# Optimization experiments

Measured on AMD Instinct MI355X. Metric: run time of the kernel, lower is better.

## Reference

```python
import jax, jax.numpy as jnp
import numpy as np

WS = 800      # window size
HEADS = 3
DH = 24       # dim_head
LOWRANK_W = 30
NEG_SLOPE = 0.01  # LeakyReLU default
LN_EPS = 1e-5


def _layernorm(x, g, b):
    m = jnp.mean(x, axis=-1, keepdims=True)
    v = jnp.var(x, axis=-1, keepdims=True)
    return (x - m) * jax.lax.rsqrt(v + LN_EPS) * g + b


def setup_inputs() -> dict:
    key = jax.random.key(0)
    ks = jax.random.split(key, 20)
    B, CIN, H, W = 2, 5, 160, 160
    D = 48
    INNER = HEADS * DH  # 72
    f32 = jnp.float32

    def n(k, shape, s=0.05):
        return jax.random.normal(k, shape, f32) * s

    return {
        "x": jax.random.normal(ks[0], (B, CIN, H, W), f32),
        # Embedding: Conv2d(5, 48, 3, pad=1) + PReLU
        "conv_w": n(ks[1], (D, CIN, 3, 3), 0.1),
        "conv_b": jnp.zeros((D,), f32),
        "prelu_a": jnp.array(0.25, f32),
        # attention PreNorm
        "ln1_g": jnp.ones((D,), f32),
        "ln1_b": jnp.zeros((D,), f32),
        # to_qkv: Linear(48, 216, bias=False)
        "w_qkv": n(ks[2], (3 * INNER, D)),
        # Linformer low-rank params E,F: [heads, dim_head, w]
        "E_mat": jax.random.normal(ks[3], (HEADS, DH, LOWRANK_W), f32),
        "F_mat": jax.random.normal(ks[4], (HEADS, DH, LOWRANK_W), f32),
        # lin1/lin2: Linear(w, dim_head)
        "w_e": n(ks[5], (DH, LOWRANK_W)),
        "b_e": jnp.zeros((DH,), f32),
        "w_f": n(ks[6], (DH, LOWRANK_W)),
        "b_f": jnp.zeros((DH,), f32),
        # to_out: Linear(72, 48)
        "w_out": n(ks[7], (D, INNER)),
        "b_out": jnp.zeros((D,), f32),
        # FF PreNorm + MLP (dim=48, hidden=48)
        "ln2_g": jnp.ones((D,), f32),
        "ln2_b": jnp.zeros((D,), f32),
        "ff_w1": n(ks[8], (D, D)),
        "ff_b1": jnp.zeros((D,), f32),
        "ff_w2": n(ks[9], (D, D)),
        "ff_b2": jnp.zeros((D,), f32),
        # final lin1: Linear(48, 96)
        "w_fin": n(ks[10], (2 * D, D)),
        "b_fin": jnp.zeros((2 * D,), f32),
    }


def reference(x, conv_w, conv_b, prelu_a, ln1_g, ln1_b, w_qkv, E_mat, F_mat,
              w_e, b_e, w_f, b_f, w_out, b_out, ln2_g, ln2_b,
              ff_w1, ff_b1, ff_w2, ff_b2, w_fin, b_fin):
    B, _, H, W = x.shape
    # Embedding: conv3x3 same + PReLU
    E = jax.lax.conv_general_dilated(
        x, conv_w, (1, 1), ((1, 1), (1, 1)),
        dimension_numbers=("NCHW", "OIHW", "NCHW")) + conv_b[None, :, None, None]
    E = jnp.maximum(E, 0) + prelu_a * jnp.minimum(E, 0)
    D = E.shape[1]
    seq = E.reshape(B, D, H * W).transpose(0, 2, 1)  # [B, N, D]
    N = seq.shape[1]
    nw = N // WS

    # --- Residual(PreNorm(LinformerAttention_wind1)) ---
    xn = _layernorm(seq, ln1_g, ln1_b)
    xw = xn.reshape(B, nw, WS, D)                         # windows
    qkv = jnp.einsum("bwnc,oc->bwno", xw, w_qkv)          # [B,nw,WS,216]
    qkv = qkv.reshape(B, nw, WS, HEADS, 3 * DH).transpose(0, 1, 3, 2, 4)
    q, k, v = jnp.split(qkv, 3, axis=-1)                  # each [B,nw,h,WS,DH]
    # einsum 'b h n d, h d d -> b h n d' == scale by diagonal of lin(E/F)
    e_diag = jnp.einsum("hdw,dw->hd", E_mat, w_e) + b_e   # [h, DH]
    f_diag = jnp.einsum("hdw,dw->hd", F_mat, w_f) + b_f
    k = k * e_diag[None, None, :, None, :]
    v = v * f_diag[None, None, :, None, :]
    scale = DH ** -0.5
    dots = jnp.einsum("bwhid,bwhjd->bwhij", q, k) * scale  # [B,nw,h,WS,WS]
    attn = jax.nn.softmax(dots, axis=-1)
    ow = jnp.einsum("bwhij,bwhjd->bwhid", attn, v)
    ow = ow.transpose(0, 1, 3, 2, 4).reshape(B, N, HEADS * DH)
    att = jnp.einsum("bnf,of->bno", ow, w_out) + b_out
    seq = seq + att

    # --- Residual(PreNorm(FeedForward)) ---
    yn = _layernorm(seq, ln2_g, ln2_b)
    h = jnp.einsum("bnc,oc->bno", yn, ff_w1) + ff_b1
    h = jnp.where(h >= 0, h, NEG_SLOPE * h)
    h = jnp.einsum("bno,co->bnc", h, ff_w2) + ff_b2
    att1 = seq + h                                        # [B, N, D]

    hp = att1.transpose(0, 2, 1).reshape(B, D, H, W)
    Highpass1 = E * hp + E
    lin = jnp.einsum("bnc,oc->bno", att1, w_fin) + b_fin  # [B, N, 2D]
    return (Highpass1, lin)
```

## Files before the change

### kernel.cpp

```cpp
#include <hip/hip_runtime.h>
#include <hip/hip_bf16.h>

#define B_    2
#define CIN_  5
#define H_    160
#define W_    160
#define N_    25600
#define D_    48
#define NW_   32
#define WS_   800
#define HEADS_ 3
#define DH_   24
#define INNER_ 72
#define NWH_  192

typedef __bf16 bf16x8 __attribute__((ext_vector_type(8)));
typedef float  f32x4  __attribute__((ext_vector_type(4)));

#define MFMA(a,b,c) __builtin_amdgcn_mfma_f32_16x16x32_bf16((a),(b),(c),0,0,0)

__device__ __forceinline__ float fast_exp2(float x) {
#if __has_builtin(__builtin_amdgcn_exp2f)
    return __builtin_amdgcn_exp2f(x);
#else
    return exp2f(x);
#endif
}

__device__ __forceinline__ unsigned pack_bf16(float lo, float hi) {
    __bf16 l = (__bf16)lo, h = (__bf16)hi;
    unsigned short ul = __builtin_bit_cast(unsigned short, l);
    unsigned short uh = __builtin_bit_cast(unsigned short, h);
    return ((unsigned)uh << 16) | (unsigned)ul;
}

__global__ __launch_bounds__(256) void k_wprep(const float* __restrict__ wqkv,
                                               const float* __restrict__ w_out,
                                               const float* __restrict__ fw1,
                                               const float* __restrict__ fw2,
                                               const float* __restrict__ wfin,
                                               const float* __restrict__ cw,
                                               const float* __restrict__ Em,
                                               const float* __restrict__ Fm,
                                               const float* __restrict__ we,
                                               const float* __restrict__ be,
                                               const float* __restrict__ wf,
                                               const float* __restrict__ bf,
                                               float* __restrict__ diag,
                                               __bf16* __restrict__ wqB,
                                               __bf16* __restrict__ woB,
                                               __bf16* __restrict__ f1B,
                                               __bf16* __restrict__ f2B,
                                               __bf16* __restrict__ wfB,
                                               __bf16* __restrict__ wcB) {
    if (blockIdx.x == 0 && threadIdx.x < 72) {
        int tt = threadIdx.x;
        int h = tt / 24, d = tt % 24;
        float se = be[d], sf = bf[d];
        for (int w = 0; w < 30; ++w) {
            se += Em[(h*24+d)*30 + w] * we[d*30 + w];
            sf += Fm[(h*24+d)*30 + w] * wf[d*30 + w];
        }
        diag[tt]      = se;
        diag[72 + tt] = sf;
    }
    int t = blockIdx.x*256 + threadIdx.x, stride = gridDim.x*256;
    for (int i = t; i < 288*64; i += stride) {
        int grow = i>>6, c = i&63;
        int gg = grow>>5, q = grow&31, tt = q>>4, sp = q&15, d = tt*16+sp;
        int part = gg/3, head = gg%3;
        wqB[i] = (d<24 && c<48) ? (__bf16)wqkv[(head*72 + part*24 + d)*48 + c] : (__bf16)0.f;
    }
    for (int i = t; i < 48*96;  i += stride) {
        int o = i/96, p = i%96;
        int h = p>>5, q = p&31, j = q&1, sp = q>>1, d = j*16+sp;
        woB[i] = (d<24) ? (__bf16)w_out[o*72 + h*24 + d] : (__bf16)0.f;
    }
    for (int i = t; i < 48*64;  i += stride) { int o=i>>6, c=i&63; f1B[i] = (c<48)? (__bf16)fw1[o*48+c] : (__bf16)0.f; }
    for (int i = t; i < 48*64;  i += stride) { int o=i>>6, c=i&63; f2B[i] = (c<48)? (__bf16)fw2[o*48+c] : (__bf16)0.f; }
    for (int i = t; i < 96*64;  i += stride) { int o=i>>6, c=i&63; wfB[i] = (c<48)? (__bf16)wfin[o*48+c] : (__bf16)0.f; }
    for (int i = t; i < 48*64;  i += stride) { int o=i>>6, c=i&63; wcB[i] = (c<45)? (__bf16)cw[o*45+c] : (__bf16)0.f; }
}

__global__ __launch_bounds__(256) void k_cqkv(const float* __restrict__ x,
                                              const __bf16* __restrict__ wcB,
                                              const float* __restrict__ cb,
                                              const float* __restrict__ pa,
                                              const __bf16* __restrict__ wqB,
                                              const float* __restrict__ g1,
                                              const float* __restrict__ b1,
                                              const float* __restrict__ diag,
                                              float* __restrict__ seqT,
                                              __bf16* __restrict__ Qbf,
                                              __bf16* __restrict__ Kbf,
                                              __bf16* __restrict__ Vt) {
    __shared__ float Lx[CIN_][4][W_];
    __shared__ __bf16 xfer[64*64];
    int t = threadIdx.x;
    int blk = blockIdx.x;
    int b = blk / 400;
    int n0 = (blk % 400) * 64;
    int y0 = n0 / W_;

    for (int i = t; i < CIN_*4*W_; i += 256) {
        int ic = i / (4*W_), rem = i % (4*W_), yy = rem / W_, col = rem % W_;
        int yr = y0 - 1 + yy;
        float v = 0.f;
        if (yr >= 0 && yr < H_)
            v = x[((size_t)(b*CIN_ + ic)*H_ + yr)*W_ + col];
        Lx[ic][yy][col] = v;
    }
    __syncthreads();

    int wv = t >> 6, lane = t & 63, g = lane>>4, s = lane&15;
    char* xb = (char*)xfer;

    {
        int rloc0 = wv * 16;
        bf16x8 ac[2];
        {
            int row = rloc0 + s;
            int n  = n0 + row;
            int y  = n / W_, xx = n % W_;
            int dy = y - y0;
            #pragma unroll
            for (int kc = 0; kc < 2; ++kc) {
                int kbase = kc*32 + g*8;
                #pragma unroll
                for (int j = 0; j < 8; ++j) {
                    int k = kbase + j;
                    int ic = k / 9, rem = k % 9, ky = rem / 3, kx = rem % 3;
                    int xc = xx + kx - 1;
                    float v = 0.f;
                    if ((kc == 0 || k < 45) && xc >= 0 && xc < W_)
                        v = Lx[ic][dy + ky][xc];
                    ac[kc][j] = (__bf16)v;
                }
            }
        }
        const bf16x8* WC4 = (const bf16x8*)wcB;
        float a = pa[0];
        float cbv[3], g1v[3], b1v[3];
        #pragma unroll
        for (int n = 0; n < 3; ++n) {
            cbv[n] = cb[n*16+s]; g1v[n] = g1[n*16+s]; b1v[n] = b1[n*16+s];
        }
        float xr[3][4];
        #pragma unroll
        for (int n = 0; n < 3; ++n) {
            bf16x8 wb0 = WC4[(n*16+s)*8 + g];
            bf16x8 wb1 = WC4[(n*16+s)*8 + 4 + g];
            f32x4 c = {0.f,0.f,0.f,0.f};
            c = MFMA(ac[0], wb0, c);
            c = MFMA(ac[1], wb1, c);
            #pragma unroll
            for (int r = 0; r < 4; ++r) {
                float vv = c[r] + cbv[n];
                vv = vv >= 0.f ? vv : a * vv;
                xr[n][r] = vv;
            }
        }
        int grow0 = blk*64 + rloc0;
        #pragma unroll
        for (int n = 0; n < 3; ++n)
          #pragma unroll
          for (int r = 0; r < 4; ++r)
            seqT[(size_t)(grow0 + g*4 + r)*48 + n*16 + s] = xr[n][r];

        #pragma unroll
        for (int r = 0; r < 4; ++r) {
            float sm = xr[0][r] + xr[1][r] + xr[2][r];
            float sq = xr[0][r]*xr[0][r] + xr[1][r]*xr[1][r] + xr[2][r]*xr[2][r];
            #pragma unroll
            for (int msk = 1; msk < 16; msk <<= 1) { sm += __shfl_xor(sm, msk); sq += __shfl_xor(sq, msk); }
            float mean = sm * (1.f/48.f);
            float var  = sq * (1.f/48.f) - mean*mean;
            float rs   = rsqrtf(var + 1e-5f);
            int row = rloc0 + g*4 + r;
            int sw  = ((g*4+r)&7) << 4;
            #pragma unroll
            for (int n = 0; n < 3; ++n) {
                float yn = (xr[n][r] - mean) * rs * g1v[n] + b1v[n];
                *(__bf16*)(xb + ((row*128 + (n*16+s)*2) ^ sw)) = (__bf16)yn;
            }
            *(__bf16*)(xb + ((row*128 + (48+s)*2) ^ sw)) = (__bf16)0.f;
        }
    }
    __syncthreads();

    int rh = wv & 1, gh = wv >> 1;
    int growQ = blk*64 + rh*32;
    int nrem = growQ % N_;
    int w = nrem / WS_, i0 = nrem % WS_;
    size_t headbase = (size_t)((b*NW_ + w)*HEADS_);

    bf16x8 af[2][2];
    #pragma unroll
    for (int m = 0; m < 2; ++m)
      #pragma unroll
      for (int kc = 0; kc < 2; ++kc) {
        int row = rh*32 + m*16 + s;
        af[m][kc] = *(const bf16x8*)(xb + ((row*128 + kc*64 + g*16) ^ ((s&7)<<4)));
      }

    const bf16x8* WQ4 = (const bf16x8*)wqB;
    const float SCALE = 0.2944889919f;

    float dke[3], dko[3], dve[3], dvo[3];
    #pragma unroll
    for (int h = 0; h < 3; ++h) {
        dke[h] = diag[h*24 + s];
        dko[h] = (s < 8) ? diag[h*24 + 16 + s] : 0.f;
        dve[h] = diag[72 + h*24 + s];
        dvo[h] = (s < 8) ? diag[72 + h*24 + 16 + s] : 0.f;
    }

    unsigned* Qd = (unsigned*)Qbf;
    unsigned* Kd = (unsigned*)Kbf;

    int gg0 = gh ? 5 : 0, gg1 = gh ? 9 : 5;
    for (int gg = gg0; gg < gg1; ++gg) {
        int part = gg / 3, head = gg % 3;
        bf16x8 we0 = WQ4[(gg*32 +      s)*8 +     g];
        bf16x8 we1 = WQ4[(gg*32 +      s)*8 + 4 + g];
        bf16x8 wo0 = WQ4[(gg*32 + 16 + s)*8 +     g];
        bf16x8 wo1 = WQ4[(gg*32 + 16 + s)*8 + 4 + g];
        f32x4 ce[2], co[2];
        __builtin_amdgcn_s_setprio(1);
        #pragma unroll
        for (int m = 0; m < 2; ++m) {
            f32x4 c = {0.f,0.f,0.f,0.f};
            c = MFMA(af[m][0], we0, c); c = MFMA(af[m][1], we1, c);
            ce[m] = c;
            f32x4 d = {0.f,0.f,0.f,0.f};
            d = MFMA(af[m][0], wo0, d); d = MFMA(af[m][1], wo1, d);
            co[m] = d;
        }
        __builtin_amdgcn_s_setprio(0);
        size_t rbase = (headbase + head)*WS_ + i0;
        if (part == 0) {
            #pragma unroll
            for (int m = 0; m < 2; ++m)
              #pragma unroll
              for (int r = 0; r < 4; ++r)
                Qd[(rbase + m*16 + g*4 + r)*16 + s] =
                    pack_bf16(ce[m][r]*SCALE, co[m][r]*SCALE);
        } else if (part == 1) {
            #pragma unroll
            for (int m = 0; m < 2; ++m)
              #pragma unroll
              for (int r = 0; r < 4; ++r) {
                int p5 = 16*(g&1) + 8*m + 4*(g>>1) + r;
                Kd[(rbase + p5)*16 + s] =
                    pack_bf16(ce[m][r]*dke[head], co[m][r]*dko[head]);
              }
        } else {
            size_t vbase = (headbase + head)*((size_t)32*WS_) + i0;
            #pragma unroll
            for (int m = 0; m < 2; ++m) {
                uint2 pe;
                pe.x = pack_bf16(ce[m][0]*dve[head], ce[m][1]*dve[head]);
                pe.y = pack_bf16(ce[m][2]*dve[head], ce[m][3]*dve[head]);
                *(uint2*)&Vt[vbase + (size_t)s*WS_ + m*16 + g*4] = pe;
                if (s < 8) {
                    uint2 po;
                    po.x = pack_bf16(co[m][0]*dvo[head], co[m][1]*dvo[head]);
                    po.y = pack_bf16(co[m][2]*dvo[head], co[m][3]*dvo[head]);
                    *(uint2*)&Vt[vbase + (size_t)(16+s)*WS_ + m*16 + g*4] = po;
                }
            }
        }
    }
    if (gh == 1) {
        unsigned* Vd = (unsigned*)Vt;
        #pragma unroll
        for (int it = 0; it < 6; ++it) {
            int idx = it*64 + lane;
            int h = idx >> 7, rem = idx & 127;
            int dd = 24 + (rem >> 4), cp = rem & 15;
            size_t ubase = (((headbase + h)*((size_t)32*WS_) + (size_t)dd*WS_ + i0) >> 1);
            Vd[ubase + cp] = (dd == 24) ? 0x3F803F80u : 0u;
        }
    }
}

__global__ __launch_bounds__(256, 4) void k_attn(const __bf16* __restrict__ Qbf,
                                                 const __bf16* __restrict__ Kbf,
                                                 const __bf16* __restrict__ Vt,
                                                 __bf16* __restrict__ OW) {
    __shared__ float red[2][5][2][4][64];
    int t = threadIdx.x;
    int wv = t >> 6, lane = t & 63;
    int g = lane >> 4, s = lane & 15;
    int half = wv & 1, tsk = wv >> 1;
    int blk = blockIdx.x;
    int v = (blk & 7) * 120 + (blk >> 3);
    int task = v * 2 + tsk;
    int wh = task / 10, qt = task % 10;
    int q0 = qt * 80;

    const bf16x8* Qp = (const bf16x8*)(Qbf + ((size_t)wh*WS_ + q0)*32);
    const bf16x8* Kp = (const bf16x8*)(Kbf + (size_t)wh*WS_*32);
    const bf16x8* Vp = (const bf16x8*)(Vt  + (size_t)wh*32*WS_);

    bf16x8 qb[5];
    #pragma unroll
    for (int i = 0; i < 5; ++i) qb[i] = Qp[(i*16 + s)*4 + g];

    f32x4 o[5][2];
    #pragma unroll
    for (int i = 0; i < 5; ++i) {
        o[i][0] = (f32x4){0.f,0.f,0.f,0.f};
        o[i][1] = (f32x4){0.f,0.f,0.f,0.f};
    }

    int c0 = half ? 12 : 0;
    int c1 = half ? 25 : 12;

    bf16x8 ka0 = Kp[(c0*32 + s)*4 + g];
    bf16x8 ka1 = Kp[(c0*32 + 16 + s)*4 + g];
    bf16x8 vb0 = Vp[s*100 + c0*4 + g];
    bf16x8 vb1 = Vp[(16+s)*100 + c0*4 + g];

    for (int c = c0; c < c1; ++c) {
        int cn = (c + 1 < c1) ? c + 1 : c0;
        bf16x8 nk0 = Kp[(cn*32 + s)*4 + g];
        bf16x8 nk1 = Kp[(cn*32 + 16 + s)*4 + g];
        bf16x8 nv0 = Vp[s*100 + cn*4 + g];
        bf16x8 nv1 = Vp[(16+s)*100 + cn*4 + g];

        __builtin_amdgcn_s_setprio(1);
        #pragma unroll
        for (int i = 0; i < 5; ++i) {
            f32x4 s0 = {0.f,0.f,0.f,0.f}, s1 = {0.f,0.f,0.f,0.f};
            s0 = MFMA(ka0, qb[i], s0);
            s1 = MFMA(ka1, qb[i], s1);
            bf16x8 pa;
            #pragma unroll
            for (int r = 0; r < 4; ++r) {
                pa[r]     = (__bf16)fast_exp2(s0[r]);
                pa[r + 4] = (__bf16)fast_exp2(s1[r]);
            }
            o[i][0] = MFMA(pa, vb0, o[i][0]);
            o[i][1] = MFMA(pa, vb1, o[i][1]);
        }
        __builtin_amdgcn_s_setprio(0);
        ka0 = nk0; ka1 = nk1; vb0 = nv0; vb1 = nv1;
    }

    if (half) {
        #pragma unroll
        for (int i = 0; i < 5; ++i)
          #pragma unroll
          for (int j = 0; j < 2; ++j)
            #pragma unroll
            for (int r = 0; r < 4; ++r)
              red[tsk][i][j][r][lane] = o[i][j][r];
    }
    __syncthreads();
    if (!half) {
        #pragma unroll
        for (int i = 0; i < 5; ++i)
          #pragma unroll
          for (int j = 0; j < 2; ++j)
            #pragma unroll
            for (int r = 0; r < 4; ++r)
              o[i][j][r] += red[tsk][i][j][r][lane];

        int bw = wh / 3, h = wh % 3;
        int b = bw >> 5, w = bw & 31;
        unsigned* OWd = (unsigned*)OW;
        #pragma unroll
        for (int i = 0; i < 5; ++i) {
            #pragma unroll
            for (int r = 0; r < 4; ++r) {
                float den = __shfl(o[i][1][r], (lane & 48) + 8);
                float inv = 1.f / den;
                int n = w*WS_ + q0 + i*16 + g*4 + r;
                OWd[(size_t)(b*N_ + n)*48 + h*16 + s] =
                    pack_bf16(o[i][0][r]*inv, o[i][1][r]*inv);
            }
        }
    }
}

__global__ __launch_bounds__(256) void k_tail(const float* __restrict__ seqT,
                                              const __bf16* __restrict__ OW,
                                              const __bf16* __restrict__ woB,
                                              const float* __restrict__ b_out,
                                              const float* __restrict__ g2,
                                              const float* __restrict__ b2,
                                              const __bf16* __restrict__ f1B,
                                              const float* __restrict__ fb1,
                                              const __bf16* __restrict__ f2B,
                                              const float* __restrict__ fb2,
                                              const __bf16* __restrict__ wfB,
                                              const float* __restrict__ bfin,
                                              float* __restrict__ out1,
                                              float* __restrict__ out2) {
    __shared__ __bf16 xfer[4][2048];
    __shared__ float hp[4][32][49];
    int t = threadIdx.x, wv = t>>6, lane = t&63, g = lane>>4, s = lane&15;
    int row0 = (blockIdx.x*4 + wv) * 32;
    char* xb = (char*)&xfer[wv][0];

    int b = row0 / N_;
    int nbase = row0 % N_;

    const bf16x8* OW4 = (const bf16x8*)OW;
    const bf16x8* WO4 = (const bf16x8*)woB;
    const bf16x8* F14 = (const bf16x8*)f1B;
    const bf16x8* F24 = (const bf16x8*)f2B;
    const bf16x8* WF4 = (const bf16x8*)wfB;

    bf16x8 aow[2][3];
    #pragma unroll
    for (int m = 0; m < 2; ++m)
      #pragma unroll
      for (int kc = 0; kc < 3; ++kc)
        aow[m][kc] = OW4[(size_t)(row0 + m*16 + s)*12 + kc*4 + g];

    f32x4 s2[2][3];
    __builtin_amdgcn_s_setprio(1);
    #pragma unroll
    for (int n = 0; n < 3; ++n) {
        bf16x8 wb0 = WO4[(n*16+s)*12 + g];
        bf16x8 wb1 = WO4[(n*16+s)*12 + 4 + g];
        bf16x8 wb2 = WO4[(n*16+s)*12 + 8 + g];
        #pragma unroll
        for (int m = 0; m < 2; ++m) {
            f32x4 c = {0.f,0.f,0.f,0.f};
            c = MFMA(aow[m][0], wb0, c);
            c = MFMA(aow[m][1], wb1, c);
            c = MFMA(aow[m][2], wb2, c);
            s2[m][n] = c;
        }
    }
    __builtin_amdgcn_s_setprio(0);
    float bov[3], g2v[3], b2v[3], f1bv[3], f2bv[3];
    #pragma unroll
    for (int n = 0; n < 3; ++n) {
        bov[n] = b_out[n*16+s]; g2v[n] = g2[n*16+s]; b2v[n] = b2[n*16+s];
        f1bv[n] = fb1[n*16+s];  f2bv[n] = fb2[n*16+s];
    }
    float sv[2][3][4];
    #pragma unroll
    for (int m = 0; m < 2; ++m)
      #pragma unroll
      for (int n = 0; n < 3; ++n)
        #pragma unroll
        for (int r = 0; r < 4; ++r) {
          sv[m][n][r] = seqT[(size_t)(row0 + m*16 + g*4 + r)*48 + n*16 + s];
          s2[m][n][r] += sv[m][n][r] + bov[n];
        }

    #pragma unroll
    for (int m = 0; m < 2; ++m)
      #pragma unroll
      for (int r = 0; r < 4; ++r) {
        float sm = s2[m][0][r] + s2[m][1][r] + s2[m][2][r];
        float sq = s2[m][0][r]*s2[m][0][r] + s2[m][1][r]*s2[m][1][r] + s2[m][2][r]*s2[m][2][r];
        #pragma unroll
        for (int msk = 1; msk < 16; msk <<= 1) { sm += __shfl_xor(sm, msk); sq += __shfl_xor(sq, msk); }
        float mean = sm * (1.f/48.f);
        float var  = sq * (1.f/48.f) - mean*mean;
        float rs   = rsqrtf(var + 1e-5f);
        int row = m*16 + g*4 + r;
        int sw  = ((g*4+r)&7) << 4;
        #pragma unroll
        for (int n = 0; n < 3; ++n) {
            float yn = (s2[m][n][r] - mean) * rs * g2v[n] + b2v[n];
            *(__bf16*)(xb + ((row*128 + (n*16+s)*2) ^ sw)) = (__bf16)yn;
        }
        *(__bf16*)(xb + ((row*128 + (48+s)*2) ^ sw)) = (__bf16)0.f;
      }

    bf16x8 af[2][2];
    f32x4 hh[2][3];

    #pragma unroll
    for (int m = 0; m < 2; ++m)
      #pragma unroll
      for (int kc = 0; kc < 2; ++kc)
        af[m][kc] = *(const bf16x8*)(xb + (((m*16+s)*128 + kc*64 + g*16) ^ ((s&7)<<4)));
    __builtin_amdgcn_s_setprio(1);
    #pragma unroll
    for (int n = 0; n < 3; ++n) {
        bf16x8 wb0 = F14[(n*16+s)*8 + g];
        bf16x8 wb1 = F14[(n*16+s)*8 + 4 + g];
        #pragma unroll
        for (int m = 0; m < 2; ++m) {
            f32x4 c = {0.f,0.f,0.f,0.f};
            c = MFMA(af[m][0], wb0, c);
            c = MFMA(af[m][1], wb1, c);
            hh[m][n] = c;
        }
    }
    __builtin_amdgcn_s_setprio(0);
    #pragma unroll
    for (int m = 0; m < 2; ++m)
      #pragma unroll
      for (int r = 0; r < 4; ++r) {
        int row = m*16 + g*4 + r;
        int sw  = ((g*4+r)&7) << 4;
        #pragma unroll
        for (int n = 0; n < 3; ++n) {
            float v = hh[m][n][r] + f1bv[n];
            v = v >= 0.f ? v : 0.01f*v;
            *(__bf16*)(xb + ((row*128 + (n*16+s)*2) ^ sw)) = (__bf16)v;
        }
        *(__bf16*)(xb + ((row*128 + (48+s)*2) ^ sw)) = (__bf16)0.f;
      }

    #pragma unroll
    for (int m = 0; m < 2; ++m)
      #pragma unroll
      for (int kc = 0; kc < 2; ++kc)
        af[m][kc] = *(const bf16x8*)(xb + (((m*16+s)*128 + kc*64 + g*16) ^ ((s&7)<<4)));
    __builtin_amdgcn_s_setprio(1);
    #pragma unroll
    for (int n = 0; n < 3; ++n) {
        bf16x8 wb0 = F24[(n*16+s)*8 + g];
        bf16x8 wb1 = F24[(n*16+s)*8 + 4 + g];
        #pragma unroll
        for (int m = 0; m < 2; ++m) {
            f32x4 c = {0.f,0.f,0.f,0.f};
            c = MFMA(af[m][0], wb0, c);
            c = MFMA(af[m][1], wb1, c);
            hh[m][n] = c;
        }
    }
    __builtin_amdgcn_s_setprio(0);
    #pragma unroll
    for (int m = 0; m < 2; ++m)
      #pragma unroll
      for (int r = 0; r < 4; ++r) {
        int row = m*16 + g*4 + r;
        int sw  = ((g*4+r)&7) << 4;
        #pragma unroll
        for (int n = 0; n < 3; ++n) {
            float a1v = s2[m][n][r] + hh[m][n][r] + f2bv[n];
            hp[wv][row][n*16+s] = sv[m][n][r] * (1.f + a1v);
            *(__bf16*)(xb + ((row*128 + (n*16+s)*2) ^ sw)) = (__bf16)a1v;
        }
        *(__bf16*)(xb + ((row*128 + (48+s)*2) ^ sw)) = (__bf16)0.f;
      }

    #pragma unroll
    for (int it = 0; it < 6; ++it) {
        int flat = it*256 + lane*4;
        int ch = flat >> 5, row = flat & 31;
        float4 v = { hp[wv][row][ch], hp[wv][row+1][ch],
                     hp[wv][row+2][ch], hp[wv][row+3][ch] };
        *(float4*)&out1[((size_t)b*D_ + ch)*N_ + nbase + row] = v;
    }

    #pragma unroll
    for (int m = 0; m < 2; ++m)
      #pragma unroll
      for (int kc = 0; kc < 2; ++kc)
        af[m][kc] = *(const bf16x8*)(xb + (((m*16+s)*128 + kc*64 + g*16) ^ ((s&7)<<4)));
    #pragma unroll
    for (int n = 0; n < 6; ++n) {
        bf16x8 wb0 = WF4[(n*16+s)*8 + g];
        bf16x8 wb1 = WF4[(n*16+s)*8 + 4 + g];
        float bfv = bfin[n*16+s];
        __builtin_amdgcn_s_setprio(1);
        f32x4 cc[2];
        #pragma unroll
        for (int m = 0; m < 2; ++m) {
            f32x4 c = {0.f,0.f,0.f,0.f};
            c = MFMA(af[m][0], wb0, c);
            c = MFMA(af[m][1], wb1, c);
            cc[m] = c;
        }
        __builtin_amdgcn_s_setprio(0);
        #pragma unroll
        for (int m = 0; m < 2; ++m)
          #pragma unroll
          for (int r = 0; r < 4; ++r)
            out2[(size_t)(row0 + m*16 + g*4 + r)*96 + n*16 + s] = cc[m][r] + bfv;
    }
}

extern "C" void kernel_launch(void* const* d_in, const int* in_sizes, int n_in,
                              void* d_out, int out_size, void* d_ws, size_t ws_size,
                              hipStream_t stream) {
    const float* x      = (const float*)d_in[0];
    const float* conv_w = (const float*)d_in[1];
    const float* conv_b = (const float*)d_in[2];
    const float* prelu_a= (const float*)d_in[3];
    const float* ln1_g  = (const float*)d_in[4];
    const float* ln1_b  = (const float*)d_in[5];
    const float* w_qkv  = (const float*)d_in[6];
    const float* E_mat  = (const float*)d_in[7];
    const float* F_mat  = (const float*)d_in[8];
    const float* w_e    = (const float*)d_in[9];
    const float* b_e    = (const float*)d_in[10];
    const float* w_f    = (const float*)d_in[11];
    const float* b_f    = (const float*)d_in[12];
    const float* w_out  = (const float*)d_in[13];
    const float* b_out  = (const float*)d_in[14];
    const float* ln2_g  = (const float*)d_in[15];
    const float* ln2_b  = (const float*)d_in[16];
    const float* ff_w1  = (const float*)d_in[17];
    const float* ff_b1  = (const float*)d_in[18];
    const float* ff_w2  = (const float*)d_in[19];
    const float* ff_b2  = (const float*)d_in[20];
    const float* w_fin  = (const float*)d_in[21];
    const float* b_fin  = (const float*)d_in[22];

    float* ws = (float*)d_ws;
    float*  seqT = ws;
    float*  diag = seqT + (size_t)B_*N_*D_;
    __bf16* Qbf  = (__bf16*)(diag + 144);
    __bf16* Kbf  = Qbf + (size_t)NWH_*WS_*32;
    __bf16* Vt   = Kbf + (size_t)NWH_*WS_*32;
    __bf16* OW   = Vt + (size_t)NWH_*32*WS_;
    __bf16* wqB  = OW + (size_t)B_*N_*96;
    __bf16* woB  = wqB + 288*64;
    __bf16* f1B  = woB + 48*96;
    __bf16* f2B  = f1B + 48*64;
    __bf16* wfB  = f2B + 48*64;
    __bf16* wcB  = wfB + 96*64;

    float* out1 = (float*)d_out;
    float* out2 = out1 + (size_t)B_*D_*N_;

    k_wprep<<<32, 256, 0, stream>>>(w_qkv, w_out, ff_w1, ff_w2, w_fin, conv_w,
                                    E_mat, F_mat, w_e, b_e, w_f, b_f, diag,
                                    wqB, woB, f1B, f2B, wfB, wcB);
    k_cqkv<<<800, 256, 0, stream>>>(x, wcB, conv_b, prelu_a,
                                    wqB, ln1_g, ln1_b, diag, seqT, Qbf, Kbf, Vt);
    k_attn<<<960, 256, 0, stream>>>(Qbf, Kbf, Vt, OW);
    k_tail<<<400, 256, 0, stream>>>(seqT, OW, woB, b_out, ln2_g, ln2_b,
                                    f1B, ff_b1, f2B, ff_b2, wfB, b_fin,
                                    out1, out2);
}
```

Before: 72.69 us.

## Split tail kernel output columns across three waves per row tile

Restructures k_tail so each 32-row tile is processed by three waves, each owning one 16-column slice of the 48 output channels, instead of one wave doing all columns. LayerNorm row statistics are combined through a small shared buffer, and double shared staging buffers with block barriers replace per-wave private buffers. The launch grows to 800 blocks of 384 threads. This aims to raise parallelism and cut per-wave serial MFMA and epilogue work. In exchange it adds __syncthreads barriers and redundant loads of the activation fragments in every wave.

```diff
diff --git a/kernel.cpp b/kernel.cpp
--- a/kernel.cpp
+++ b/kernel.cpp
@@ -384,7 +384,7 @@
     }
 }
 
-__global__ __launch_bounds__(256) void k_tail(const float* __restrict__ seqT,
+__global__ __launch_bounds__(384) void k_tail(const float* __restrict__ seqT,
                                               const __bf16* __restrict__ OW,
                                               const __bf16* __restrict__ woB,
                                               const float* __restrict__ b_out,
@@ -398,14 +398,19 @@
                                               const float* __restrict__ bfin,
                                               float* __restrict__ out1,
                                               float* __restrict__ out2) {
-    __shared__ __bf16 xfer[4][2048];
-    __shared__ float hp[4][32][49];
-    int t = threadIdx.x, wv = t>>6, lane = t&63, g = lane>>4, s = lane&15;
-    int row0 = (blockIdx.x*4 + wv) * 32;
-    char* xb = (char*)&xfer[wv][0];
-
+    __shared__ __bf16 xA[2][2048];
+    __shared__ __bf16 xB[2][2048];
+    __shared__ float  hp[2][32][49];
+    __shared__ float  lnp[2][3][2][32];
+    int t = threadIdx.x;
+    int w6 = t / 64, lane = t & 63, g = lane >> 4, s = lane & 15;
+    int rh = w6 / 3, nc = w6 % 3;
+    int blk = blockIdx.x;
+    int row0 = blk*64 + rh*32;
     int b = row0 / N_;
-    int nbase = row0 % N_;
+    int nbase0 = (blk*64) % N_;
+    char* xa  = (char*)&xA[rh][0];
+    char* xbb = (char*)&xB[rh][0];
 
     const bf16x8* OW4 = (const bf16x8*)OW;
     const bf16x8* WO4 = (const bf16x8*)woB;
@@ -420,153 +425,159 @@
       for (int kc = 0; kc < 3; ++kc)
         aow[m][kc] = OW4[(size_t)(row0 + m*16 + s)*12 + kc*4 + g];
 
-    f32x4 s2[2][3];
-    __builtin_amdgcn_s_setprio(1);
-    #pragma unroll
-    for (int n = 0; n < 3; ++n) {
-        bf16x8 wb0 = WO4[(n*16+s)*12 + g];
-        bf16x8 wb1 = WO4[(n*16+s)*12 + 4 + g];
-        bf16x8 wb2 = WO4[(n*16+s)*12 + 8 + g];
+    f32x4 s2[2];
+    {
+        bf16x8 wb0 = WO4[(nc*16+s)*12 + g];
+        bf16x8 wb1 = WO4[(nc*16+s)*12 + 4 + g];
+        bf16x8 wb2 = WO4[(nc*16+s)*12 + 8 + g];
+        __builtin_amdgcn_s_setprio(1);
         #pragma unroll
         for (int m = 0; m < 2; ++m) {
             f32x4 c = {0.f,0.f,0.f,0.f};
             c = MFMA(aow[m][0], wb0, c);
             c = MFMA(aow[m][1], wb1, c);
             c = MFMA(aow[m][2], wb2, c);
-            s2[m][n] = c;
-        }
-    }
-    __builtin_amdgcn_s_setprio(0);
-    float bov[3], g2v[3], b2v[3], f1bv[3], f2bv[3];
-    #pragma unroll
-    for (int n = 0; n < 3; ++n) {
-        bov[n] = b_out[n*16+s]; g2v[n] = g2[n*16+s]; b2v[n] = b2[n*16+s];
-        f1bv[n] = fb1[n*16+s];  f2bv[n] = fb2[n*16+s];
-    }
-    float sv[2][3][4];
-    #pragma unroll
-    for (int m = 0; m < 2; ++m)
-      #pragma unroll
-      for (int n = 0; n < 3; ++n)
-        #pragma unroll
-        for (int r = 0; r < 4; ++r) {
-          sv[m][n][r] = seqT[(size_t)(row0 + m*16 + g*4 + r)*48 + n*16 + s];
-          s2[m][n][r] += sv[m][n][r] + bov[n];
-        }
-
+            s2[m] = c;
+        }
+        __builtin_amdgcn_s_setprio(0);
+    }
+    float bov  = b_out[nc*16+s];
+    float g2v  = g2[nc*16+s],  b2v  = b2[nc*16+s];
+    float f1bv = fb1[nc*16+s], f2bv = fb2[nc*16+s];
+
+    float sv[2][4];
     #pragma unroll
     for (int m = 0; m < 2; ++m)
       #pragma unroll
       for (int r = 0; r < 4; ++r) {
-        float sm = s2[m][0][r] + s2[m][1][r] + s2[m][2][r];
-        float sq = s2[m][0][r]*s2[m][0][r] + s2[m][1][r]*s2[m][1][r] + s2[m][2][r]*s2[m][2][r];
+        sv[m][r] = seqT[(size_t)(row0 + m*16 + g*4 + r)*48 + nc*16 + s];
+        s2[m][r] += sv[m][r] + bov;
+      }
+
+    #pragma unroll
+    for (int m = 0; m < 2; ++m)
+      #pragma unroll
+      for (int r = 0; r < 4; ++r) {
+        float sm = s2[m][r];
+        float sq = s2[m][r]*s2[m][r];
         #pragma unroll
         for (int msk = 1; msk < 16; msk <<= 1) { sm += __shfl_xor(sm, msk); sq += __shfl_xor(sq, msk); }
+        if (s == 0) {
+            int row = m*16 + g*4 + r;
+            lnp[rh][nc][0][row] = sm;
+            lnp[rh][nc][1][row] = sq;
+        }
+      }
+    __syncthreads();
+
+    #pragma unroll
+    for (int m = 0; m < 2; ++m)
+      #pragma unroll
+      for (int r = 0; r < 4; ++r) {
+        int row = m*16 + g*4 + r;
+        float sm = lnp[rh][0][0][row] + lnp[rh][1][0][row] + lnp[rh][2][0][row];
+        float sq = lnp[rh][0][1][row] + lnp[rh][1][1][row] + lnp[rh][2][1][row];
         float mean = sm * (1.f/48.f);
         float var  = sq * (1.f/48.f) - mean*mean;
         float rs   = rsqrtf(var + 1e-5f);
-        int row = m*16 + g*4 + r;
-        int sw  = ((g*4+r)&7) << 4;
-        #pragma unroll
-        for (int n = 0; n < 3; ++n) {
-            float yn = (s2[m][n][r] - mean) * rs * g2v[n] + b2v[n];
-            *(__bf16*)(xb + ((row*128 + (n*16+s)*2) ^ sw)) = (__bf16)yn;
-        }
-        *(__bf16*)(xb + ((row*128 + (48+s)*2) ^ sw)) = (__bf16)0.f;
+        float yn = (s2[m][r] - mean) * rs * g2v + b2v;
+        int sw = ((g*4+r)&7) << 4;
+        *(__bf16*)(xa + ((row*128 + (nc*16+s)*2) ^ sw)) = (__bf16)yn;
+        if (nc == 0)
+            *(__bf16*)(xa + ((row*128 + (48+s)*2) ^ sw)) = (__bf16)0.f;
       }
+    __syncthreads();
 
     bf16x8 af[2][2];
-    f32x4 hh[2][3];
+    f32x4 hh[2];
 
     #pragma unroll
     for (int m = 0; m < 2; ++m)
       #pragma unroll
       for (int kc = 0; kc < 2; ++kc)
-        af[m][kc] = *(const bf16x8*)(xb + (((m*16+s)*128 + kc*64 + g*16) ^ ((s&7)<<4)));
-    __builtin_amdgcn_s_setprio(1);
-    #pragma unroll
-    for (int n = 0; n < 3; ++n) {
-        bf16x8 wb0 = F14[(n*16+s)*8 + g];
-        bf16x8 wb1 = F14[(n*16+s)*8 + 4 + g];
+        af[m][kc] = *(const bf16x8*)(xa + (((m*16+s)*128 + kc*64 + g*16) ^ ((s&7)<<4)));
+    {
+        bf16x8 wb0 = F14[(nc*16+s)*8 + g];
+        bf16x8 wb1 = F14[(nc*16+s)*8 + 4 + g];
+        __builtin_amdgcn_s_setprio(1);
         #pragma unroll
         for (int m = 0; m < 2; ++m) {
             f32x4 c = {0.f,0.f,0.f,0.f};
             c = MFMA(af[m][0], wb0, c);
             c = MFMA(af[m][1], wb1, c);
-            hh[m][n] = c;
-        }
-    }
-    __builtin_amdgcn_s_setprio(0);
+            hh[m] = c;
+        }
+        __builtin_amdgcn_s_setprio(0);
+    }
     #pragma unroll
     for (int m = 0; m < 2; ++m)
       #pragma unroll
       for (int r = 0; r < 4; ++r) {
         int row = m*16 + g*4 + r;
         int sw  = ((g*4+r)&7) << 4;
-        #pragma unroll
-        for (int n = 0; n < 3; ++n) {
-            float v = hh[m][n][r] + f1bv[n];
-            v = v >= 0.f ? v : 0.01f*v;
-            *(__bf16*)(xb + ((row*128 + (n*16+s)*2) ^ sw)) = (__bf16)v;
-        }
-        *(__bf16*)(xb + ((row*128 + (48+s)*2) ^ sw)) = (__bf16)0.f;
+        float v = hh[m][r] + f1bv;
+        v = v >= 0.f ? v : 0.01f*v;
+        *(__bf16*)(xbb + ((row*128 + (nc*16+s)*2) ^ sw)) = (__bf16)v;
+        if (nc == 0)
+            *(__bf16*)(xbb + ((row*128 + (48+s)*2) ^ sw)) = (__bf16)0.f;
       }
+    __syncthreads();
 
     #pragma unroll
     for (int m = 0; m < 2; ++m)
       #pragma unroll
       for (int kc = 0; kc < 2; ++kc)
-        af[m][kc] = *(const bf16x8*)(xb + (((m*16+s)*128 + kc*64 + g*16) ^ ((s&7)<<4)));
-    __builtin_amdgcn_s_setprio(1);
-    #pragma unroll
-    for (int n = 0; n < 3; ++n) {
-        bf16x8 wb0 = F24[(n*16+s)*8 + g];
-        bf16x8 wb1 = F24[(n*16+s)*8 + 4 + g];
+        af[m][kc] = *(const bf16x8*)(xbb + (((m*16+s)*128 + kc*64 + g*16) ^ ((s&7)<<4)));
+    {
+        bf16x8 wb0 = F24[(nc*16+s)*8 + g];
+        bf16x8 wb1 = F24[(nc*16+s)*8 + 4 + g];
+        __builtin_amdgcn_s_setprio(1);
         #pragma unroll
         for (int m = 0; m < 2; ++m) {
             f32x4 c = {0.f,0.f,0.f,0.f};
             c = MFMA(af[m][0], wb0, c);
             c = MFMA(af[m][1], wb1, c);
-            hh[m][n] = c;
-        }
-    }
-    __builtin_amdgcn_s_setprio(0);
+            hh[m] = c;
+        }
+        __builtin_amdgcn_s_setprio(0);
+    }
     #pragma unroll
     for (int m = 0; m < 2; ++m)
       #pragma unroll
       for (int r = 0; r < 4; ++r) {
         int row = m*16 + g*4 + r;
         int sw  = ((g*4+r)&7) << 4;
-        #pragma unroll
-        for (int n = 0; n < 3; ++n) {
-            float a1v = s2[m][n][r] + hh[m][n][r] + f2bv[n];
-            hp[wv][row][n*16+s] = sv[m][n][r] * (1.f + a1v);
-            *(__bf16*)(xb + ((row*128 + (n*16+s)*2) ^ sw)) = (__bf16)a1v;
-        }
-        *(__bf16*)(xb + ((row*128 + (48+s)*2) ^ sw)) = (__bf16)0.f;
+        float a1v = s2[m][r] + hh[m][r] + f2bv;
+        hp[rh][row][nc*16+s] = sv[m][r] * (1.f + a1v);
+        *(__bf16*)(xa + ((row*128 + (nc*16+s)*2) ^ sw)) = (__bf16)a1v;
+        if (nc == 0)
+            *(__bf16*)(xa + ((row*128 + (48+s)*2) ^ sw)) = (__bf16)0.f;
       }
-
-    #pragma unroll
-    for (int it = 0; it < 6; ++it) {
-        int flat = it*256 + lane*4;
-        int ch = flat >> 5, row = flat & 31;
-        float4 v = { hp[wv][row][ch], hp[wv][row+1][ch],
-                     hp[wv][row+2][ch], hp[wv][row+3][ch] };
-        *(float4*)&out1[((size_t)b*D_ + ch)*N_ + nbase + row] = v;
+    __syncthreads();
+
+    #pragma unroll
+    for (int it = 0; it < 2; ++it) {
+        int flat = it*1536 + t*4;
+        int ch = flat >> 6, row = flat & 63;
+        int h2 = row >> 5, rl = row & 31;
+        float4 v = { hp[h2][rl][ch], hp[h2][rl+1][ch],
+                     hp[h2][rl+2][ch], hp[h2][rl+3][ch] };
+        *(float4*)&out1[((size_t)b*D_ + ch)*N_ + nbase0 + row] = v;
     }
 
     #pragma unroll
     for (int m = 0; m < 2; ++m)
       #pragma unroll
       for (int kc = 0; kc < 2; ++kc)
-        af[m][kc] = *(const bf16x8*)(xb + (((m*16+s)*128 + kc*64 + g*16) ^ ((s&7)<<4)));
-    #pragma unroll
-    for (int n = 0; n < 6; ++n) {
+        af[m][kc] = *(const bf16x8*)(xa + (((m*16+s)*128 + kc*64 + g*16) ^ ((s&7)<<4)));
+    #pragma unroll
+    for (int nn = 0; nn < 2; ++nn) {
+        int n = nc + nn*3;
         bf16x8 wb0 = WF4[(n*16+s)*8 + g];
         bf16x8 wb1 = WF4[(n*16+s)*8 + 4 + g];
         float bfv = bfin[n*16+s];
+        f32x4 cc[2];
         __builtin_amdgcn_s_setprio(1);
-        f32x4 cc[2];
         #pragma unroll
         for (int m = 0; m < 2; ++m) {
             f32x4 c = {0.f,0.f,0.f,0.f};
@@ -633,7 +644,7 @@
     k_cqkv<<<800, 256, 0, stream>>>(x, wcB, conv_b, prelu_a,
                                     wqB, ln1_g, ln1_b, diag, seqT, Qbf, Kbf, Vt);
     k_attn<<<960, 256, 0, stream>>>(Qbf, Kbf, Vt, OW);
-    k_tail<<<400, 256, 0, stream>>>(seqT, OW, woB, b_out, ln2_g, ln2_b,
+    k_tail<<<800, 384, 0, stream>>>(seqT, OW, woB, b_out, ln2_g, ln2_b,
                                     f1B, ff_b1, f2B, ff_b2, wfB, b_fin,
                                     out1, out2);
 }
```

New measurement: 80.60 us. +10.9%, slower.

## Halve conv+QKV tile to 32 rows with narrow halo staging, doubling grid

Applied to the files above, without the earlier changes.

The fused conv/LayerNorm/QKV kernel now processes 32 tokens per block instead of 64, launching 1600 blocks. It stages only a 3x34 halo of the input per channel instead of four full image rows, which cuts redundant global loads and LDS use. The 9 QKV head-groups are redistributed across all four waves (2,2,3,2 groups), and wave 3 writes the V padding. Only two waves do the conv stage now, and each block repeats the weight loads and halo overhead.

```diff
diff --git a/kernel.cpp b/kernel.cpp
--- a/kernel.cpp
+++ b/kernel.cpp
@@ -94,20 +94,22 @@
                                               __bf16* __restrict__ Qbf,
                                               __bf16* __restrict__ Kbf,
                                               __bf16* __restrict__ Vt) {
-    __shared__ float Lx[CIN_][4][W_];
-    __shared__ __bf16 xfer[64*64];
+    __shared__ float Lx[CIN_][3][34];
+    __shared__ __bf16 xfer[32*64];
     int t = threadIdx.x;
     int blk = blockIdx.x;
-    int b = blk / 400;
-    int n0 = (blk % 400) * 64;
+    int b = blk / 800;
+    int n0 = (blk % 800) * 32;
     int y0 = n0 / W_;
-
-    for (int i = t; i < CIN_*4*W_; i += 256) {
-        int ic = i / (4*W_), rem = i % (4*W_), yy = rem / W_, col = rem % W_;
+    int x0 = n0 % W_;
+
+    for (int i = t; i < CIN_*3*34; i += 256) {
+        int ic = i / (3*34), rem = i % (3*34), yy = rem / 34, col = rem % 34;
         int yr = y0 - 1 + yy;
+        int xc = x0 - 1 + col;
         float v = 0.f;
-        if (yr >= 0 && yr < H_)
-            v = x[((size_t)(b*CIN_ + ic)*H_ + yr)*W_ + col];
+        if (yr >= 0 && yr < H_ && xc >= 0 && xc < W_)
+            v = x[((size_t)(b*CIN_ + ic)*H_ + yr)*W_ + xc];
         Lx[ic][yy][col] = v;
     }
     __syncthreads();
@@ -115,27 +117,21 @@
     int wv = t >> 6, lane = t & 63, g = lane>>4, s = lane&15;
     char* xb = (char*)xfer;
 
-    {
+    if (wv < 2) {
         int rloc0 = wv * 16;
+        int rib = rloc0 + s;
         bf16x8 ac[2];
-        {
-            int row = rloc0 + s;
-            int n  = n0 + row;
-            int y  = n / W_, xx = n % W_;
-            int dy = y - y0;
-            #pragma unroll
-            for (int kc = 0; kc < 2; ++kc) {
-                int kbase = kc*32 + g*8;
-                #pragma unroll
-                for (int j = 0; j < 8; ++j) {
-                    int k = kbase + j;
-                    int ic = k / 9, rem = k % 9, ky = rem / 3, kx = rem % 3;
-                    int xc = xx + kx - 1;
-                    float v = 0.f;
-                    if ((kc == 0 || k < 45) && xc >= 0 && xc < W_)
-                        v = Lx[ic][dy + ky][xc];
-                    ac[kc][j] = (__bf16)v;
-                }
+        #pragma unroll
+        for (int kc = 0; kc < 2; ++kc) {
+            int kbase = kc*32 + g*8;
+            #pragma unroll
+            for (int j = 0; j < 8; ++j) {
+                int k = kbase + j;
+                int ic = k / 9, rem = k % 9, ky = rem / 3, kx = rem % 3;
+                float v = 0.f;
+                if (kc == 0 || k < 45)
+                    v = Lx[ic][ky][rib + kx];
+                ac[kc][j] = (__bf16)v;
             }
         }
         const bf16x8* WC4 = (const bf16x8*)wcB;
@@ -160,7 +156,7 @@
                 xr[n][r] = vv;
             }
         }
-        int grow0 = blk*64 + rloc0;
+        int grow0 = blk*32 + rloc0;
         #pragma unroll
         for (int n = 0; n < 3; ++n)
           #pragma unroll
@@ -188,10 +184,7 @@
     }
     __syncthreads();
 
-    int rh = wv & 1, gh = wv >> 1;
-    int growQ = blk*64 + rh*32;
-    int nrem = growQ % N_;
-    int w = nrem / WS_, i0 = nrem % WS_;
+    int w = n0 / WS_, i0 = n0 % WS_;
     size_t headbase = (size_t)((b*NW_ + w)*HEADS_);
 
     bf16x8 af[2][2];
@@ -199,7 +192,7 @@
     for (int m = 0; m < 2; ++m)
       #pragma unroll
       for (int kc = 0; kc < 2; ++kc) {
-        int row = rh*32 + m*16 + s;
+        int row = m*16 + s;
         af[m][kc] = *(const bf16x8*)(xb + ((row*128 + kc*64 + g*16) ^ ((s&7)<<4)));
       }
 
@@ -218,7 +211,8 @@
     unsigned* Qd = (unsigned*)Qbf;
     unsigned* Kd = (unsigned*)Kbf;
 
-    int gg0 = gh ? 5 : 0, gg1 = gh ? 9 : 5;
+    int gg0 = (wv < 3) ? wv*2 : 7;
+    int gg1 = (wv == 2) ? 7 : gg0 + 2;
     for (int gg = gg0; gg < gg1; ++gg) {
         int part = gg / 3, head = gg % 3;
         bf16x8 we0 = WQ4[(gg*32 +      s)*8 +     g];
@@ -271,7 +265,7 @@
             }
         }
     }
-    if (gh == 1) {
+    if (wv == 3) {
         unsigned* Vd = (unsigned*)Vt;
         #pragma unroll
         for (int it = 0; it < 6; ++it) {
@@ -630,8 +624,8 @@
     k_wprep<<<32, 256, 0, stream>>>(w_qkv, w_out, ff_w1, ff_w2, w_fin, conv_w,
                                     E_mat, F_mat, w_e, b_e, w_f, b_f, diag,
                                     wqB, woB, f1B, f2B, wfB, wcB);
-    k_cqkv<<<800, 256, 0, stream>>>(x, wcB, conv_b, prelu_a,
-                                    wqB, ln1_g, ln1_b, diag, seqT, Qbf, Kbf, Vt);
+    k_cqkv<<<1600, 256, 0, stream>>>(x, wcB, conv_b, prelu_a,
+                                     wqB, ln1_g, ln1_b, diag, seqT, Qbf, Kbf, Vt);
     k_attn<<<960, 256, 0, stream>>>(Qbf, Kbf, Vt, OW);
     k_tail<<<400, 256, 0, stream>>>(seqT, OW, woB, b_out, ln2_g, ln2_b,
                                     f1B, ff_b1, f2B, ff_b2, wfB, b_fin,
```

Result: faster. 70.81 us (-2.6%).
